# Kernel tuning notes

Hardware: AMD Instinct MI355X
Metric: run time of the kernel (lower is better)

Reference implementation:

```python
import jax, jax.numpy as jnp
import numpy as np
from jax import lax

DIM = 64
HID = 256
TIME_LEN = 21  # t in [0, 1], dt = 0.05 <= h_max = 0.1 -> one RK4 step per interval
BS = 65536


def setup_inputs() -> dict:
    key = jax.random.key(0)
    k1, k2, k3 = jax.random.split(key, 3)
    z0 = jax.random.normal(k1, (BS, DIM), dtype=jnp.float32)
    t = jnp.arange(TIME_LEN, dtype=jnp.float32) * 0.05
    W1 = jax.random.normal(k2, (DIM, HID), dtype=jnp.float32) / np.sqrt(DIM)
    b1 = jnp.zeros((HID,), dtype=jnp.float32)
    W2 = jax.random.normal(k3, (HID, DIM), dtype=jnp.float32) / np.sqrt(HID)
    b2 = jnp.zeros((DIM,), dtype=jnp.float32)
    return {"z0": z0, "t": t, "W1": W1, "b1": b1, "W2": W2, "b2": b2}


def reference(z0, t, W1, b1, W2, b2):
    # ODEF dynamics: 2-layer tanh MLP, f(z, t) = tanh(z @ W1 + b1) @ W2 + b2
    def f(z, t_i):
        return jnp.tanh(z @ W1 + b1) @ W2 + b2

    # Classic RK44 step from t0 to t1 (dt <= h_max so each solve is one step),
    # matching ode_solver.solve(z0, t[i], t[i+1], func) with relaxation off.
    def step(z, t_pair):
        t0, t1 = t_pair[0], t_pair[1]
        h = t1 - t0
        k1 = f(z, t0)
        k2 = f(z + 0.5 * h * k1, t0 + 0.5 * h)
        k3 = f(z + 0.5 * h * k2, t0 + 0.5 * h)
        k4 = f(z + h * k3, t1)
        zn = z + (h / 6.0) * (k1 + 2.0 * k2 + 2.0 * k3 + k4)
        return zn, zn

    t_pairs = jnp.stack([t[:-1], t[1:]], axis=1)  # [time_len-1, 2]
    _, zs = lax.scan(step, z0, t_pairs)
    # Whole trajectory, as ODEAdjoint.forward stores: [time_len, bs, dim]
    return jnp.concatenate([z0[None], zs], axis=0)
```

## Files before the change

kernel.cpp:

```cpp
#include <hip/hip_runtime.h>

#define DIM   64
#define HID   256
#define TLEN  21
#define BS    65536
#define BLOCK 512
#define WAVES 8
#define ROWS_PER_WAVE 16
#define ROWS_PER_BLOCK 128
#define NBLOCKS (BS / ROWS_PER_BLOCK)

typedef __bf16    bf16x8   __attribute__((ext_vector_type(8)));
typedef float     f32x16   __attribute__((ext_vector_type(16)));
typedef float     f32x4    __attribute__((ext_vector_type(4)));
typedef unsigned  uint32x4 __attribute__((ext_vector_type(4)));

__device__ __forceinline__ bf16x8 as_bf16x8(uint32x4 u) {
    return __builtin_bit_cast(bf16x8, u);
}

__device__ __forceinline__ unsigned pack2(float a, float b) {
    unsigned r;
    asm("v_cvt_pk_bf16_f32 %0, %1, %2" : "=v"(r) : "v"(a), "v"(b));
    return r;
}

__device__ __forceinline__ float tanh_2x(float x) {
    float e = __builtin_amdgcn_exp2f(x);
    float r = __builtin_amdgcn_rcpf(e + 1.0f);
    return fmaf(-2.0f, r, 1.0f);
}

template<int OFF>
__device__ __forceinline__ uint32x4 ds128(unsigned base) {
    uint32x4 d;
    asm volatile("ds_read_b128 %0, %1 offset:%c2"
                 : "=v"(d) : "v"(base), "i"(OFF) : "memory");
    return d;
}
template<int K>
__device__ __forceinline__ void wait_lgkm() {
    asm volatile("s_waitcnt lgkmcnt(%c0)" :: "i"(K) : "memory");
    __builtin_amdgcn_sched_barrier(0);
}
__device__ __forceinline__ unsigned lds_base(const void* p) {
    return (unsigned)(unsigned long long)p;
}

__device__ __forceinline__ f32x4 mfma16(bf16x8 a, bf16x8 b, f32x4 c) {
    return __builtin_amdgcn_mfma_f32_16x16x32_bf16(a, b, c, 0, 0, 0);
}

struct A1Buf { uint32x4 a0, a1, a2, a3, b0, b1; };
struct A2Buf { uint32x4 a0, a1, a2, a3; };

template<int N>
__device__ __forceinline__ void issue_a1b1(unsigned a1b, unsigned b1b, A1Buf& g) {
    g.a0 = ds128<(4 * N + 0) * 1024>(a1b);
    g.a1 = ds128<(4 * N + 1) * 1024>(a1b);
    g.a2 = ds128<(4 * N + 2) * 1024>(a1b);
    g.a3 = ds128<(4 * N + 3) * 1024>(a1b);
    g.b0 = ds128<(2 * N) * 64>(b1b);
    g.b1 = ds128<(2 * N + 1) * 64>(b1b);
}
template<int N>
__device__ __forceinline__ void issue_a2(unsigned a2b, A2Buf& g) {
    g.a0 = ds128<(0 * 8 + N) * 1024>(a2b);
    g.a1 = ds128<(1 * 8 + N) * 1024>(a2b);
    g.a2 = ds128<(2 * 8 + N) * 1024>(a2b);
    g.a3 = ds128<(3 * 8 + N) * 1024>(a2b);
}

template<int N>
__device__ __forceinline__ void kt2_pipe(unsigned a1b, unsigned a2b, unsigned b1b,
                                         A1Buf& cur1, A1Buf& nxt1,
                                         A2Buf& cur2, A2Buf& nxt2,
                                         bf16x8 bk0, bf16x8 bk1,
                                         f32x4& d20, f32x4& d21,
                                         f32x4& d22, f32x4& d23)
{
    if constexpr (N < 7) issue_a1b1<N + 1>(a1b, b1b, nxt1);
    wait_lgkm<N < 7 ? 10 : 4>();
    f32x4 d1e = __builtin_bit_cast(f32x4, cur1.b0);
    f32x4 d1o = __builtin_bit_cast(f32x4, cur1.b1);
    d1e = mfma16(as_bf16x8(cur1.a0), bk0, d1e);
    d1e = mfma16(as_bf16x8(cur1.a1), bk1, d1e);
    d1o = mfma16(as_bf16x8(cur1.a2), bk0, d1o);
    d1o = mfma16(as_bf16x8(cur1.a3), bk1, d1o);

    if constexpr (N < 7) issue_a2<N + 1>(a2b, nxt2);

    uint32x4 bt;
    bt[0] = pack2(tanh_2x(d1e[0]), tanh_2x(d1e[1]));
    bt[1] = pack2(tanh_2x(d1e[2]), tanh_2x(d1e[3]));
    bt[2] = pack2(tanh_2x(d1o[0]), tanh_2x(d1o[1]));
    bt[3] = pack2(tanh_2x(d1o[2]), tanh_2x(d1o[3]));
    bf16x8 btb = as_bf16x8(bt);

    wait_lgkm<N < 7 ? 10 : 0>();
    d20 = mfma16(as_bf16x8(cur2.a0), btb, d20);
    d21 = mfma16(as_bf16x8(cur2.a1), btb, d21);
    d22 = mfma16(as_bf16x8(cur2.a2), btb, d22);
    d23 = mfma16(as_bf16x8(cur2.a3), btb, d23);
}

__device__ __forceinline__ f32x16 feval(unsigned a1b, unsigned a2b,
                                        unsigned b1b, unsigned b2b,
                                        uint32x4 bkA, uint32x4 bkB)
{
    bf16x8 bk0 = as_bf16x8(bkA);
    bf16x8 bk1 = as_bf16x8(bkB);

    uint32x4 u0 = ds128<0>(b2b);
    uint32x4 u1 = ds128<64>(b2b);
    uint32x4 u2 = ds128<128>(b2b);
    uint32x4 u3 = ds128<192>(b2b);

    A1Buf g0, g1;
    A2Buf h0, h1;
    issue_a1b1<0>(a1b, b1b, g0);
    issue_a2<0>(a2b, h0);
    wait_lgkm<10>();
    f32x4 d20 = __builtin_bit_cast(f32x4, u0);
    f32x4 d21 = __builtin_bit_cast(f32x4, u1);
    f32x4 d22 = __builtin_bit_cast(f32x4, u2);
    f32x4 d23 = __builtin_bit_cast(f32x4, u3);

    kt2_pipe<0>(a1b, a2b, b1b, g0, g1, h0, h1, bk0, bk1, d20, d21, d22, d23);
    kt2_pipe<1>(a1b, a2b, b1b, g1, g0, h1, h0, bk0, bk1, d20, d21, d22, d23);
    kt2_pipe<2>(a1b, a2b, b1b, g0, g1, h0, h1, bk0, bk1, d20, d21, d22, d23);
    kt2_pipe<3>(a1b, a2b, b1b, g1, g0, h1, h0, bk0, bk1, d20, d21, d22, d23);
    kt2_pipe<4>(a1b, a2b, b1b, g0, g1, h0, h1, bk0, bk1, d20, d21, d22, d23);
    kt2_pipe<5>(a1b, a2b, b1b, g1, g0, h1, h0, bk0, bk1, d20, d21, d22, d23);
    kt2_pipe<6>(a1b, a2b, b1b, g0, g1, h0, h1, bk0, bk1, d20, d21, d22, d23);
    kt2_pipe<7>(a1b, a2b, b1b, g1, g0, h1, h0, bk0, bk1, d20, d21, d22, d23);

    f32x16 k;
    #pragma unroll
    for (int i = 0; i < 4; i++) {
        k[i]      = d20[i];
        k[4 + i]  = d21[i];
        k[8 + i]  = d22[i];
        k[12 + i] = d23[i];
    }
    return k;
}

__device__ __forceinline__ uint32x4 pack_lo(f32x16 v) {
    uint32x4 r;
    r[0] = pack2(v[0], v[1]); r[1] = pack2(v[2], v[3]);
    r[2] = pack2(v[4], v[5]); r[3] = pack2(v[6], v[7]);
    return r;
}
__device__ __forceinline__ uint32x4 pack_hi(f32x16 v) {
    uint32x4 r;
    r[0] = pack2(v[8], v[9]);   r[1] = pack2(v[10], v[11]);
    r[2] = pack2(v[12], v[13]); r[3] = pack2(v[14], v[15]);
    return r;
}
__device__ __forceinline__ uint32x4 packaxpy_lo(float c, f32x16 k, f32x16 z) {
    uint32x4 r;
    r[0] = pack2(fmaf(c, k[0], z[0]), fmaf(c, k[1], z[1]));
    r[1] = pack2(fmaf(c, k[2], z[2]), fmaf(c, k[3], z[3]));
    r[2] = pack2(fmaf(c, k[4], z[4]), fmaf(c, k[5], z[5]));
    r[3] = pack2(fmaf(c, k[6], z[6]), fmaf(c, k[7], z[7]));
    return r;
}
__device__ __forceinline__ uint32x4 packaxpy_hi(float c, f32x16 k, f32x16 z) {
    uint32x4 r;
    r[0] = pack2(fmaf(c, k[8],  z[8]),  fmaf(c, k[9],  z[9]));
    r[1] = pack2(fmaf(c, k[10], z[10]), fmaf(c, k[11], z[11]));
    r[2] = pack2(fmaf(c, k[12], z[12]), fmaf(c, k[13], z[13]));
    r[3] = pack2(fmaf(c, k[14], z[14]), fmaf(c, k[15], z[15]));
    return r;
}
__device__ __forceinline__ f32x16 axpy16(float c, f32x16 k, f32x16 z) {
    f32x16 r;
    #pragma unroll
    for (int i = 0; i < 16; i++) r[i] = fmaf(c, k[i], z[i]);
    return r;
}

extern "C" __global__ __launch_bounds__(BLOCK, 1) void node_mfma_kernel(
    const float* __restrict__ z0, const float* __restrict__ tarr,
    const float* __restrict__ W1, const float* __restrict__ b1,
    const float* __restrict__ W2, const float* __restrict__ b2,
    float* __restrict__ out)
{
    __shared__ __align__(16) unsigned short sA1[32 * 64 * 8];
    __shared__ __align__(16) unsigned short sA2[32 * 64 * 8];
    __shared__ __align__(16) float sb1[HID];
    __shared__ __align__(16) float sb2[DIM];

    const int tid  = threadIdx.x;
    const int lane = tid & 63;
    const int wv   = tid >> 6;
    const int q    = lane >> 4;
    const int bcol = lane & 15;

    const float SC = 2.8853900817779268f;

    for (int idx = tid; idx < DIM * HID; idx += BLOCK) {
        int hid = idx & (HID - 1);
        int dim = idx >> 8;
        int ht = hid >> 4, row = hid & 15;
        int kt = dim >> 5, dlo = dim & 31;
        int j  = (dlo & 3) | ((dlo >> 4) << 2);
        int qq = (dlo >> 2) & 3;
        __bf16 bv = (__bf16)(SC * W1[idx]);
        sA1[((ht * 2 + kt) * 64 + qq * 16 + row) * 8 + j] =
            __builtin_bit_cast(unsigned short, bv);
    }
    for (int idx = tid; idx < HID * DIM; idx += BLOCK) {
        int dim = idx & (DIM - 1);
        int hid = idx >> 6;
        int mt  = dim >> 4, row = dim & 15;
        int kt2 = hid >> 5, hlo = hid & 31;
        int j   = (hlo & 3) | ((hlo >> 4) << 2);
        int qq  = (hlo >> 2) & 3;
        __bf16 bv = (__bf16)W2[idx];
        sA2[((mt * 8 + kt2) * 64 + qq * 16 + row) * 8 + j] =
            __builtin_bit_cast(unsigned short, bv);
    }
    if (tid < HID) sb1[tid] = SC * b1[tid];
    if (tid < DIM) sb2[tid] = b2[tid];

    {
        const f32x4* src = reinterpret_cast<const f32x4*>(z0 + (size_t)blockIdx.x * ROWS_PER_BLOCK * DIM);
        f32x4*       dst = reinterpret_cast<f32x4*>(out + (size_t)blockIdx.x * ROWS_PER_BLOCK * DIM);
        for (int i = tid; i < ROWS_PER_BLOCK * DIM / 4; i += BLOCK) dst[i] = src[i];
    }

    __syncthreads();

    const int rowbase = blockIdx.x * ROWS_PER_BLOCK + wv * ROWS_PER_WAVE;
    const size_t myrow = (size_t)(rowbase + bcol) * DIM;

    const unsigned a1b = lds_base(sA1) + lane * 16;
    const unsigned a2b = lds_base(sA2) + lane * 16;
    const unsigned b1b = lds_base(sb1) + q * 16;
    const unsigned b2b = lds_base(sb2) + q * 16;

    f32x16 za;
    #pragma unroll
    for (int mt = 0; mt < 4; mt++) {
        f32x4 v = *reinterpret_cast<const f32x4*>(z0 + myrow + mt * 16 + 4 * q);
        za[mt * 4 + 0] = v[0]; za[mt * 4 + 1] = v[1];
        za[mt * 4 + 2] = v[2]; za[mt * 4 + 3] = v[3];
    }

    #pragma unroll 1
    for (int s = 0; s < TLEN - 1; s++) {
        const float h  = tarr[s + 1] - tarr[s];
        const float h2 = 0.5f * h;
        const float h3 = h * (1.0f / 3.0f);
        const float h6 = h * (1.0f / 6.0f);

        f32x16 k1 = feval(a1b, a2b, b1b, b2b, pack_lo(za), pack_hi(za));
        f32x16 zf = axpy16(h6, k1, za);

        f32x16 k2 = feval(a1b, a2b, b1b, b2b,
                          packaxpy_lo(h2, k1, za), packaxpy_hi(h2, k1, za));
        zf = axpy16(h3, k2, zf);

        f32x16 k3 = feval(a1b, a2b, b1b, b2b,
                          packaxpy_lo(h2, k2, za), packaxpy_hi(h2, k2, za));
        zf = axpy16(h3, k3, zf);

        f32x16 k4 = feval(a1b, a2b, b1b, b2b,
                          packaxpy_lo(h, k3, za), packaxpy_hi(h, k3, za));
        za = axpy16(h6, k4, zf);

        float* obase = out + (size_t)(s + 1) * BS * DIM + myrow;
        #pragma unroll
        for (int mt = 0; mt < 4; mt++) {
            f32x4 v;
            v[0] = za[mt * 4 + 0]; v[1] = za[mt * 4 + 1];
            v[2] = za[mt * 4 + 2]; v[3] = za[mt * 4 + 3];
            *reinterpret_cast<f32x4*>(obase + mt * 16 + 4 * q) = v;
        }
    }
}

extern "C" void kernel_launch(void* const* d_in, const int* in_sizes, int n_in,
                              void* d_out, int out_size, void* d_ws, size_t ws_size,
                              hipStream_t stream) {
    const float* z0 = (const float*)d_in[0];
    const float* t  = (const float*)d_in[1];
    const float* W1 = (const float*)d_in[2];
    const float* b1 = (const float*)d_in[3];
    const float* W2 = (const float*)d_in[4];
    const float* b2 = (const float*)d_in[5];
    float* out = (float*)d_out;

    node_mfma_kernel<<<dim3(NBLOCKS), dim3(BLOCK), 0, stream>>>(
        z0, t, W1, b1, W2, b2, out);
}
```

Measured before the change: 433.6 us.

## Software-pipeline feval so layer-1 MFMAs overlap tanh of previous chunk

Restructures the inner hidden-chunk loop of the MLP evaluation into a skewed software pipeline. Layer-1 MFMAs for chunk N+1 and LDS prefetch of chunk N+2 are issued while the tanh/pack of chunk N and the layer-2 MFMAs of chunk N-1 proceed. The aim is to hide MFMA latency behind transcendental VALU work instead of serialising MFMA, tanh and MFMA within each chunk. This keeps more accumulators and prefetch buffers live, which raises register pressure. The new LDS wait counts also have to match the reordered issue pattern exactly.

```diff
diff --git a/kernel.cpp b/kernel.cpp
--- a/kernel.cpp
+++ b/kernel.cpp
@@ -72,36 +72,40 @@
 }
 
 template<int N>
-__device__ __forceinline__ void kt2_pipe(unsigned a1b, unsigned a2b, unsigned b1b,
-                                         A1Buf& cur1, A1Buf& nxt1,
-                                         A2Buf& cur2, A2Buf& nxt2,
-                                         bf16x8 bk0, bf16x8 bk1,
-                                         f32x4& d20, f32x4& d21,
-                                         f32x4& d22, f32x4& d23)
+__device__ __forceinline__ void iter_pipe(unsigned a1b, unsigned a2b, unsigned b1b,
+                                          A1Buf& rdA1, A1Buf& wrA1,
+                                          A2Buf& rdA2, A2Buf& wrA2,
+                                          f32x4& d1eP, f32x4& d1oP,
+                                          f32x4& d1eN, f32x4& d1oN,
+                                          bf16x8 bk0, bf16x8 bk1,
+                                          bf16x8& btbP,
+                                          f32x4& d20, f32x4& d21,
+                                          f32x4& d22, f32x4& d23)
 {
-    if constexpr (N < 7) issue_a1b1<N + 1>(a1b, b1b, nxt1);
-    wait_lgkm<N < 7 ? 10 : 4>();
-    f32x4 d1e = __builtin_bit_cast(f32x4, cur1.b0);
-    f32x4 d1o = __builtin_bit_cast(f32x4, cur1.b1);
-    d1e = mfma16(as_bf16x8(cur1.a0), bk0, d1e);
-    d1e = mfma16(as_bf16x8(cur1.a1), bk1, d1e);
-    d1o = mfma16(as_bf16x8(cur1.a2), bk0, d1o);
-    d1o = mfma16(as_bf16x8(cur1.a3), bk1, d1o);
-
-    if constexpr (N < 7) issue_a2<N + 1>(a2b, nxt2);
-
+    if constexpr (N <= 6) {
+        wait_lgkm<4>();
+        d1eN = __builtin_bit_cast(f32x4, rdA1.b0);
+        d1oN = __builtin_bit_cast(f32x4, rdA1.b1);
+        d1eN = mfma16(as_bf16x8(rdA1.a0), bk0, d1eN);
+        d1eN = mfma16(as_bf16x8(rdA1.a1), bk1, d1eN);
+        d1oN = mfma16(as_bf16x8(rdA1.a2), bk0, d1oN);
+        d1oN = mfma16(as_bf16x8(rdA1.a3), bk1, d1oN);
+    }
+    if constexpr (N <= 5) issue_a1b1<N + 2>(a1b, b1b, wrA1);
+    if constexpr (N <= 5) wait_lgkm<6>(); else wait_lgkm<0>();
+    if constexpr (N >= 1) {
+        d20 = mfma16(as_bf16x8(rdA2.a0), btbP, d20);
+        d21 = mfma16(as_bf16x8(rdA2.a1), btbP, d21);
+        d22 = mfma16(as_bf16x8(rdA2.a2), btbP, d22);
+        d23 = mfma16(as_bf16x8(rdA2.a3), btbP, d23);
+    }
+    if constexpr (N <= 6) issue_a2<N + 1>(a2b, wrA2);
     uint32x4 bt;
-    bt[0] = pack2(tanh_2x(d1e[0]), tanh_2x(d1e[1]));
-    bt[1] = pack2(tanh_2x(d1e[2]), tanh_2x(d1e[3]));
-    bt[2] = pack2(tanh_2x(d1o[0]), tanh_2x(d1o[1]));
-    bt[3] = pack2(tanh_2x(d1o[2]), tanh_2x(d1o[3]));
-    bf16x8 btb = as_bf16x8(bt);
-
-    wait_lgkm<N < 7 ? 10 : 0>();
-    d20 = mfma16(as_bf16x8(cur2.a0), btb, d20);
-    d21 = mfma16(as_bf16x8(cur2.a1), btb, d21);
-    d22 = mfma16(as_bf16x8(cur2.a2), btb, d22);
-    d23 = mfma16(as_bf16x8(cur2.a3), btb, d23);
+    bt[0] = pack2(tanh_2x(d1eP[0]), tanh_2x(d1eP[1]));
+    bt[1] = pack2(tanh_2x(d1eP[2]), tanh_2x(d1eP[3]));
+    bt[2] = pack2(tanh_2x(d1oP[0]), tanh_2x(d1oP[1]));
+    bt[3] = pack2(tanh_2x(d1oP[2]), tanh_2x(d1oP[3]));
+    btbP = as_bf16x8(bt);
 }
 
 __device__ __forceinline__ f32x16 feval(unsigned a1b, unsigned a2b,
@@ -119,21 +123,37 @@
     A1Buf g0, g1;
     A2Buf h0, h1;
     issue_a1b1<0>(a1b, b1b, g0);
-    issue_a2<0>(a2b, h0);
-    wait_lgkm<10>();
+    wait_lgkm<6>();
     f32x4 d20 = __builtin_bit_cast(f32x4, u0);
     f32x4 d21 = __builtin_bit_cast(f32x4, u1);
     f32x4 d22 = __builtin_bit_cast(f32x4, u2);
     f32x4 d23 = __builtin_bit_cast(f32x4, u3);
-
-    kt2_pipe<0>(a1b, a2b, b1b, g0, g1, h0, h1, bk0, bk1, d20, d21, d22, d23);
-    kt2_pipe<1>(a1b, a2b, b1b, g1, g0, h1, h0, bk0, bk1, d20, d21, d22, d23);
-    kt2_pipe<2>(a1b, a2b, b1b, g0, g1, h0, h1, bk0, bk1, d20, d21, d22, d23);
-    kt2_pipe<3>(a1b, a2b, b1b, g1, g0, h1, h0, bk0, bk1, d20, d21, d22, d23);
-    kt2_pipe<4>(a1b, a2b, b1b, g0, g1, h0, h1, bk0, bk1, d20, d21, d22, d23);
-    kt2_pipe<5>(a1b, a2b, b1b, g1, g0, h1, h0, bk0, bk1, d20, d21, d22, d23);
-    kt2_pipe<6>(a1b, a2b, b1b, g0, g1, h0, h1, bk0, bk1, d20, d21, d22, d23);
-    kt2_pipe<7>(a1b, a2b, b1b, g1, g0, h1, h0, bk0, bk1, d20, d21, d22, d23);
+    wait_lgkm<0>();
+    f32x4 d1eA = __builtin_bit_cast(f32x4, g0.b0);
+    f32x4 d1oA = __builtin_bit_cast(f32x4, g0.b1);
+    d1eA = mfma16(as_bf16x8(g0.a0), bk0, d1eA);
+    d1eA = mfma16(as_bf16x8(g0.a1), bk1, d1eA);
+    d1oA = mfma16(as_bf16x8(g0.a2), bk0, d1oA);
+    d1oA = mfma16(as_bf16x8(g0.a3), bk1, d1oA);
+    issue_a1b1<1>(a1b, b1b, g1);
+    issue_a2<0>(a2b, h0);
+
+    f32x4 d1eB, d1oB;
+    bf16x8 btbP = bk0;
+
+    iter_pipe<0>(a1b, a2b, b1b, g1, g0, h1, h1, d1eA, d1oA, d1eB, d1oB, bk0, bk1, btbP, d20, d21, d22, d23);
+    iter_pipe<1>(a1b, a2b, b1b, g0, g1, h0, h0, d1eB, d1oB, d1eA, d1oA, bk0, bk1, btbP, d20, d21, d22, d23);
+    iter_pipe<2>(a1b, a2b, b1b, g1, g0, h1, h1, d1eA, d1oA, d1eB, d1oB, bk0, bk1, btbP, d20, d21, d22, d23);
+    iter_pipe<3>(a1b, a2b, b1b, g0, g1, h0, h0, d1eB, d1oB, d1eA, d1oA, bk0, bk1, btbP, d20, d21, d22, d23);
+    iter_pipe<4>(a1b, a2b, b1b, g1, g0, h1, h1, d1eA, d1oA, d1eB, d1oB, bk0, bk1, btbP, d20, d21, d22, d23);
+    iter_pipe<5>(a1b, a2b, b1b, g0, g1, h0, h0, d1eB, d1oB, d1eA, d1oA, bk0, bk1, btbP, d20, d21, d22, d23);
+    iter_pipe<6>(a1b, a2b, b1b, g1, g0, h1, h1, d1eA, d1oA, d1eB, d1oB, bk0, bk1, btbP, d20, d21, d22, d23);
+    iter_pipe<7>(a1b, a2b, b1b, g0, g1, h0, h0, d1eB, d1oB, d1eA, d1oA, bk0, bk1, btbP, d20, d21, d22, d23);
+
+    d20 = mfma16(as_bf16x8(h1.a0), btbP, d20);
+    d21 = mfma16(as_bf16x8(h1.a1), btbP, d21);
+    d22 = mfma16(as_bf16x8(h1.a2), btbP, d22);
+    d23 = mfma16(as_bf16x8(h1.a3), btbP, d23);
 
     f32x16 k;
     #pragma unroll
```

Result: no change. 441.9 us (+1.9%).
